# Kernel tuning notes

Measured on AMD Instinct MI355X. Metric: run time of the kernel, lower is better.

## Reference

```python
import jax, jax.numpy as jnp
import numpy as np

N = 100000      # nodes
E = 1600000     # edges (before self-loops)
F_IN = 128      # num_feats
H = 128         # dim_hidden
C = 64          # num_classes
EPS = 1e-5      # BatchNorm eps
SLOPE = 0.2     # LeakyReLU negative slope (PyG GATConv default)


def setup_inputs() -> dict:
    key = jax.random.key(0)
    ks = jax.random.split(key, 8)
    x = jax.random.normal(ks[0], (N, F_IN), jnp.float32)
    edge_index = jax.random.randint(ks[1], (2, E), 0, N, dtype=jnp.int32)
    W0 = jax.random.normal(ks[2], (F_IN, H), jnp.float32) * (1.0 / np.sqrt(F_IN))
    a_src0 = jax.random.normal(ks[3], (H,), jnp.float32) * 0.1
    a_dst0 = jax.random.normal(ks[4], (H,), jnp.float32) * 0.1
    W1 = jax.random.normal(ks[5], (H, C), jnp.float32) * (1.0 / np.sqrt(H))
    a_src1 = jax.random.normal(ks[6], (C,), jnp.float32) * 0.1
    a_dst1 = jax.random.normal(ks[7], (C,), jnp.float32) * 0.1
    return {
        "x": x, "edge_index": edge_index,
        "W0": W0, "a_src0": a_src0, "a_dst0": a_dst0,
        "g0": jnp.ones((H,), jnp.float32), "b0": jnp.zeros((H,), jnp.float32),
        "W1": W1, "a_src1": a_src1, "a_dst1": a_dst1,
        "g1": jnp.ones((C,), jnp.float32), "b1": jnp.zeros((C,), jnp.float32),
    }


def _gat_conv(x, src, dst, W, a_s, a_d):
    # x: [N, d_in]; src/dst: [E'] (self-loops included). heads=1, bias=False.
    h = x @ W                                   # [N, d_out]
    s = h @ a_s                                 # [N] alpha_src per node
    d = h @ a_d                                 # [N] alpha_dst per node
    logits = jax.nn.leaky_relu(s[src] + d[dst], SLOPE)   # [E']
    # segment softmax over incoming edges of each dst node
    m = jax.ops.segment_max(logits, dst, num_segments=N)
    w = jnp.exp(logits - m[dst])
    denom = jax.ops.segment_sum(w, dst, num_segments=N)
    coef = w / denom[dst]                       # [E']
    return jax.ops.segment_sum(coef[:, None] * h[src], dst, num_segments=N)


def _batch_norm(x, g, b):
    mu = jnp.mean(x, axis=0)
    var = jnp.var(x, axis=0)
    return (x - mu) * jax.lax.rsqrt(var + EPS) * g + b


def reference(x, edge_index, W0, a_src0, a_dst0, g0, b0, W1, a_src1, a_dst1, g1, b1):
    loops = jnp.arange(N, dtype=edge_index.dtype)
    src = jnp.concatenate([edge_index[0], loops])
    dst = jnp.concatenate([edge_index[1], loops])
    h = _gat_conv(x, src, dst, W0, a_src0, a_dst0)
    h = jax.nn.relu(_batch_norm(h, g0, b0))
    h = _gat_conv(h, src, dst, W1, a_src1, a_dst1)
    return jax.nn.relu(_batch_norm(h, g1, b1))
```

## Files before the change

kernel.cpp:

```cpp
#include <hip/hip_runtime.h>
#include <hip/hip_bf16.h>
#include <cmath>

#define BN_EPS 1e-5f
#define SLOPE 0.2f

typedef __attribute__((ext_vector_type(8))) short bf16x8;
typedef __attribute__((ext_vector_type(4))) float f32x4;

__device__ __forceinline__ float lrelu(float x) { return x >= 0.f ? x : SLOPE * x; }
__device__ __forceinline__ float bfl(unsigned u) { return __uint_as_float(u << 16); }
__device__ __forceinline__ float bfh(unsigned u) { return __uint_as_float(u & 0xffff0000u); }
__device__ __forceinline__ float bf2f(unsigned short u) { return __uint_as_float((unsigned)u << 16); }
__device__ __forceinline__ unsigned short f2bf(float f) {
    __hip_bfloat16 h = __float2bfloat16(f);
    return *reinterpret_cast<unsigned short*>(&h);
}

__global__ __launch_bounds__(512) void k_hist(const int* __restrict__ ei, int E, int n,
                                              int nbk, int* __restrict__ gcnt) {
    __shared__ int h[512];
    int t = threadIdx.x;
    for (int i = t; i < nbk; i += 512) h[i] = 0;
    __syncthreads();
    int base = blockIdx.x * 8192;
    int tot = E + n;
#pragma unroll
    for (int k = 0; k < 16; ++k) {
        int i = base + k * 512 + t;
        if (i < tot) {
            int dst = (i < E) ? ei[E + i] : (i - E);
            atomicAdd(&h[dst >> 8], 1);
        }
    }
    __syncthreads();
    for (int i = t; i < nbk; i += 512)
        if (h[i]) atomicAdd(&gcnt[i], h[i]);
}

__global__ __launch_bounds__(512) void k_bscan(const int* __restrict__ gcnt,
                                               int* __restrict__ gbase,
                                               int* __restrict__ gnext, int nbk) {
    __shared__ int tmp[512];
    int t = threadIdx.x;
    int v = (t < nbk) ? gcnt[t] : 0;
    tmp[t] = v;
    __syncthreads();
    for (int off = 1; off < 512; off <<= 1) {
        int a = (t >= off) ? tmp[t - off] : 0;
        __syncthreads();
        tmp[t] += a;
        __syncthreads();
    }
    int ex = tmp[t] - v;
    if (t < nbk) { gbase[t] = ex; gnext[t] = ex; }
    if (t == nbk - 1) gbase[nbk] = tmp[t];
}

__global__ __launch_bounds__(512) void k_bucket(const int* __restrict__ ei, int E, int n,
                                                int nbk, int* __restrict__ gnext,
                                                int2* __restrict__ bbuf) {
    __shared__ int h[512], off[512];
    int t = threadIdx.x;
    for (int i = t; i < nbk; i += 512) h[i] = 0;
    __syncthreads();
    int base = blockIdx.x * 8192;
    int tot = E + n;
    int srcv[16], dstv[16], rnk[16];
#pragma unroll
    for (int k = 0; k < 16; ++k) {
        int i = base + k * 512 + t;
        dstv[k] = -1;
        if (i < tot) {
            int s, d;
            if (i < E) { s = ei[i]; d = ei[E + i]; }
            else       { s = i - E; d = s; }
            srcv[k] = s; dstv[k] = d;
            rnk[k] = atomicAdd(&h[d >> 8], 1);
        }
    }
    __syncthreads();
    for (int i = t; i < nbk; i += 512)
        if (h[i]) off[i] = atomicAdd(&gnext[i], h[i]);
    __syncthreads();
#pragma unroll
    for (int k = 0; k < 16; ++k) {
        int d = dstv[k];
        if (d >= 0)
            bbuf[off[d >> 8] + rnk[k]] = make_int2(srcv[k], d);
    }
}

__global__ __launch_bounds__(256) void k_csr2(const int2* __restrict__ bbuf,
                                              const int* __restrict__ gbase,
                                              int* __restrict__ rowp, int* __restrict__ csr,
                                              int* __restrict__ dste, int n, int nbk) {
    __shared__ int cnt[256], scn[256];
    int b = blockIdx.x;
    int t = threadIdx.x;
    int beg = gbase[b], end = gbase[b + 1];
    int node0 = b << 8;
    cnt[t] = 0;
    __syncthreads();
    for (int i = beg + t; i < end; i += 256)
        atomicAdd(&cnt[bbuf[i].y & 255], 1);
    __syncthreads();
    int v = cnt[t];
    scn[t] = v;
    __syncthreads();
    for (int off = 1; off < 256; off <<= 1) {
        int a = (t >= off) ? scn[t - off] : 0;
        __syncthreads();
        scn[t] += a;
        __syncthreads();
    }
    int ex = scn[t] - v;
    if (node0 + t < n) rowp[node0 + t] = beg + ex;
    if (b == nbk - 1 && t == 0) rowp[n] = end;
    cnt[t] = ex;
    __syncthreads();
    for (int i = beg + t; i < end; i += 256) {
        int2 e = bbuf[i];
        int pos = atomicAdd(&cnt[e.y & 255], 1);
        csr[beg + pos] = e.x;
        dste[beg + pos] = e.y;
    }
}

__global__ __launch_bounds__(256) void k_coef(const int* __restrict__ csr,
                                              const int* __restrict__ dste,
                                              const float* __restrict__ s,
                                              const float* __restrict__ d,
                                              float* __restrict__ wv, int tot) {
    int e4 = (blockIdx.x * 256 + threadIdx.x) * 4;
    if (e4 + 3 < tot) {
        int4 c = *(const int4*)&csr[e4];
        int4 dd = *(const int4*)&dste[e4];
        float4 w;
        w.x = __expf(lrelu(s[c.x] + d[dd.x]));
        w.y = __expf(lrelu(s[c.y] + d[dd.y]));
        w.z = __expf(lrelu(s[c.z] + d[dd.z]));
        w.w = __expf(lrelu(s[c.w] + d[dd.w]));
        *(float4*)&wv[e4] = w;
    } else {
        for (int e = e4; e < tot; ++e)
            wv[e] = __expf(lrelu(s[csr[e]] + d[dste[e]]));
    }
}

__global__ void k_packw2(const float* __restrict__ W0, const float* __restrict__ W1,
                         unsigned short* __restrict__ Wp0, unsigned short* __restrict__ Wp1) {
    int idx = blockIdx.x * 256 + threadIdx.x;
    if (idx < 128 * 128) {
        int k = idx >> 7, nG = idx & 127;
        int nt = nG >> 4, nn = nG & 15, ks = k >> 5, g = (k >> 3) & 3, j = k & 7;
        Wp0[(((nt * 4 + ks) * 64) + g * 16 + nn) * 8 + j] = f2bf(W0[idx]);
    } else {
        int i2 = idx - 128 * 128;
        if (i2 < 128 * 64) {
            int k = i2 >> 6, nG = i2 & 63;
            int nt = nG >> 4, nn = nG & 15, ks = k >> 5, g = (k >> 3) & 3, j = k & 7;
            Wp1[(((nt * 4 + ks) * 64) + g * 16 + nn) * 8 + j] = f2bf(W1[i2]);
        }
    }
}

template <int CD, bool BN_IN, bool XBF>
__global__ __launch_bounds__(256) void k_gemm_mfma(
    const void* __restrict__ Xv, const unsigned short* __restrict__ Wp,
    const float* __restrict__ bnsums, const float* __restrict__ gg,
    const float* __restrict__ bb, const float* __restrict__ a_s,
    const float* __restrict__ a_d, unsigned short* __restrict__ hb,
    float* __restrict__ s_out, float* __restrict__ d_out, int n) {
    constexpr int NT = CD / 16;
    const float* Xf = (const float*)Xv;
    const unsigned short* Xh = (const unsigned short*)Xv;
    __shared__ unsigned short wl[128 * CD];
    __shared__ float sc[128], sh[128];
    int t = threadIdx.x;
    for (int i = t * 8; i < 128 * CD; i += 2048)
        *(uint4*)&wl[i] = *(const uint4*)&Wp[i];
    if constexpr (BN_IN) {
        if (t < 128) {
            float invn = 1.f / (float)n;
            float mu = bnsums[t] * invn;
            float var = bnsums[128 + t] * invn - mu * mu;
            float s = gg[t] * rsqrtf(var + BN_EPS);
            sc[t] = s;
            sh[t] = bb[t] - mu * s;
        }
    }
    __syncthreads();
    int w = t >> 6, l = t & 63;
    int m = l & 15, g = l >> 4;
    int r0 = blockIdx.x * 64;
    int row = r0 + w * 16 + m;
    bool rv = row < n;
    bf16x8 af[4];
#pragma unroll
    for (int ks = 0; ks < 4; ++ks) {
        int c0 = ks * 32 + g * 8;
        float xv[8];
        if constexpr (XBF) {
            uint4 u = make_uint4(0, 0, 0, 0);
            if (rv) u = *(const uint4*)&Xh[(size_t)row * 128 + c0];
            unsigned uu[4] = {u.x, u.y, u.z, u.w};
#pragma unroll
            for (int q = 0; q < 4; ++q) { xv[2 * q] = bfl(uu[q]); xv[2 * q + 1] = bfh(uu[q]); }
        } else {
            float4 x0 = make_float4(0.f, 0.f, 0.f, 0.f), x1 = x0;
            if (rv) {
                x0 = *(const float4*)&Xf[(size_t)row * 128 + c0];
                x1 = *(const float4*)&Xf[(size_t)row * 128 + c0 + 4];
            }
            xv[0] = x0.x; xv[1] = x0.y; xv[2] = x0.z; xv[3] = x0.w;
            xv[4] = x1.x; xv[5] = x1.y; xv[6] = x1.z; xv[7] = x1.w;
        }
        bf16x8 a;
#pragma unroll
        for (int j = 0; j < 8; ++j) {
            float v = xv[j];
            if constexpr (BN_IN) v = fmaxf(0.f, v * sc[c0 + j] + sh[c0 + j]);
            a[j] = (short)f2bf(v);
        }
        af[ks] = a;
    }
    f32x4 acc[NT];
#pragma unroll
    for (int i = 0; i < NT; ++i) acc[i] = (f32x4){0.f, 0.f, 0.f, 0.f};
#pragma unroll
    for (int ks = 0; ks < 4; ++ks) {
#pragma unroll
        for (int nt = 0; nt < NT; ++nt) {
            bf16x8 bfr = *(bf16x8*)&wl[(((nt * 4 + ks) * 64) + l) * 8];
            acc[nt] = __builtin_amdgcn_mfma_f32_16x16x32_bf16(af[ks], bfr, acc[nt], 0, 0, 0);
        }
    }
    float ps[4] = {0.f, 0.f, 0.f, 0.f}, pd[4] = {0.f, 0.f, 0.f, 0.f};
#pragma unroll
    for (int nt = 0; nt < NT; ++nt) {
        float as = a_s[nt * 16 + m], ad = a_d[nt * 16 + m];
#pragma unroll
        for (int r = 0; r < 4; ++r) {
            ps[r] += acc[nt][r] * as;
            pd[r] += acc[nt][r] * ad;
        }
    }
#pragma unroll
    for (int off = 1; off < 16; off <<= 1) {
#pragma unroll
        for (int r = 0; r < 4; ++r) {
            ps[r] += __shfl_xor(ps[r], off);
            pd[r] += __shfl_xor(pd[r], off);
        }
    }
    __syncthreads();
    unsigned short* ot = wl;
#pragma unroll
    for (int nt = 0; nt < NT; ++nt) {
#pragma unroll
        for (int r = 0; r < 4; ++r)
            ot[(w * 16 + g * 4 + r) * CD + nt * 16 + m] = f2bf(acc[nt][r]);
    }
    if (m == 0) {
        int orow = r0 + w * 16 + g * 4;
#pragma unroll
        for (int r = 0; r < 4; ++r) {
            if (orow + r < n) { s_out[orow + r] = ps[r]; d_out[orow + r] = pd[r]; }
        }
    }
    __syncthreads();
    constexpr int CPR = CD / 8;
    for (int c = t; c < 64 * CPR; c += 256) {
        int rr = c / CPR, cc = c % CPR;
        if (r0 + rr < n)
            *(uint4*)&hb[(size_t)(r0 + rr) * CD + cc * 8] = *(uint4*)&ot[rr * CD + cc * 8];
    }
}

template <int DIM, bool OUT_BF>
__global__ __launch_bounds__(256) void k_agg(
    const unsigned short* __restrict__ hb, const float* __restrict__ wv,
    const int* __restrict__ rowp, const int* __restrict__ csr,
    void* __restrict__ outv, int n) {
    constexpr int LPE = DIM / 8;
    int gid = blockIdx.x * blockDim.x + threadIdx.x;
    int wid = gid / LPE;
    int ll = gid & (LPE - 1);
    if (wid >= n) return;
    int beg = rowp[wid], end = rowp[wid + 1];
    float acc[8] = {};
    float denom = 0.f;
    int e = beg;
    for (; e + 3 < end; e += 4) {
        int i0 = csr[e], i1 = csr[e + 1], i2 = csr[e + 2], i3 = csr[e + 3];
        float w0 = wv[e], w1 = wv[e + 1], w2 = wv[e + 2], w3 = wv[e + 3];
        uint4 p0 = *(const uint4*)&hb[(size_t)i0 * DIM + ll * 8];
        uint4 p1 = *(const uint4*)&hb[(size_t)i1 * DIM + ll * 8];
        uint4 p2 = *(const uint4*)&hb[(size_t)i2 * DIM + ll * 8];
        uint4 p3 = *(const uint4*)&hb[(size_t)i3 * DIM + ll * 8];
        denom += (w0 + w1) + (w2 + w3);
        unsigned a0[4] = {p0.x, p0.y, p0.z, p0.w};
        unsigned a1[4] = {p1.x, p1.y, p1.z, p1.w};
        unsigned a2[4] = {p2.x, p2.y, p2.z, p2.w};
        unsigned a3[4] = {p3.x, p3.y, p3.z, p3.w};
#pragma unroll
        for (int q = 0; q < 4; ++q) {
            acc[2 * q]     += w0 * bfl(a0[q]) + w1 * bfl(a1[q]) + w2 * bfl(a2[q]) + w3 * bfl(a3[q]);
            acc[2 * q + 1] += w0 * bfh(a0[q]) + w1 * bfh(a1[q]) + w2 * bfh(a2[q]) + w3 * bfh(a3[q]);
        }
    }
    for (; e < end; ++e) {
        int i0 = csr[e];
        float w0 = wv[e];
        uint4 p0 = *(const uint4*)&hb[(size_t)i0 * DIM + ll * 8];
        unsigned a0[4] = {p0.x, p0.y, p0.z, p0.w};
        denom += w0;
#pragma unroll
        for (int q = 0; q < 4; ++q) {
            acc[2 * q]     += w0 * bfl(a0[q]);
            acc[2 * q + 1] += w0 * bfh(a0[q]);
        }
    }
    float inv = 1.f / denom;
    if constexpr (OUT_BF) {
        unsigned u[4];
#pragma unroll
        for (int q = 0; q < 4; ++q)
            u[q] = (unsigned)f2bf(acc[2 * q] * inv) |
                   ((unsigned)f2bf(acc[2 * q + 1] * inv) << 16);
        *(uint4*)((unsigned short*)outv + (size_t)wid * DIM + ll * 8) =
            make_uint4(u[0], u[1], u[2], u[3]);
    } else {
        float* orow = (float*)outv + (size_t)wid * DIM + ll * 8;
        *(float4*)&orow[0] = make_float4(acc[0] * inv, acc[1] * inv, acc[2] * inv, acc[3] * inv);
        *(float4*)&orow[4] = make_float4(acc[4] * inv, acc[5] * inv, acc[6] * inv, acc[7] * inv);
    }
}

template <int CD, bool XBF>
__global__ void k_bn_stats(const void* __restrict__ xv, float* __restrict__ sums, int n) {
    const float* xf = (const float*)xv;
    const unsigned short* xh = (const unsigned short*)xv;
    constexpr int RPB = 256 / CD;
    int t = threadIdx.x;
    int c = t & (CD - 1);
    int rl = t / CD;
    float s = 0.f, sq = 0.f;
    for (int r = blockIdx.x * RPB + rl; r < n; r += gridDim.x * RPB) {
        float v = XBF ? bf2f(xh[(size_t)r * CD + c]) : xf[(size_t)r * CD + c];
        s += v;
        sq += v * v;
    }
    __shared__ float ls[256], lq[256];
    ls[t] = s; lq[t] = sq;
    __syncthreads();
    if (t < CD) {
#pragma unroll
        for (int j = 1; j < RPB; ++j) { s += ls[t + j * CD]; sq += lq[t + j * CD]; }
        atomicAdd(&sums[c], s);
        atomicAdd(&sums[CD + c], sq);
    }
}

template <int CD>
__global__ void k_bn_apply(const float* __restrict__ x, const float* __restrict__ sums,
                           const float* __restrict__ g, const float* __restrict__ b,
                           float* __restrict__ out, int n) {
    size_t i = (size_t)blockIdx.x * blockDim.x + threadIdx.x;
    size_t tot = (size_t)n * CD;
    if (i >= tot) return;
    int c = (int)(i & (CD - 1));
    float invn = 1.f / (float)n;
    float mu = sums[c] * invn;
    float var = sums[CD + c] * invn - mu * mu;
    float v = (x[i] - mu) * rsqrtf(var + BN_EPS) * g[c] + b[c];
    out[i] = fmaxf(v, 0.f);
}

extern "C" void kernel_launch(void* const* d_in, const int* in_sizes, int n_in,
                              void* d_out, int out_size, void* d_ws, size_t ws_size,
                              hipStream_t stream) {
    const float* x   = (const float*)d_in[0];
    const int*   ei  = (const int*)  d_in[1];
    const float* W0  = (const float*)d_in[2];
    const float* as0 = (const float*)d_in[3];
    const float* ad0 = (const float*)d_in[4];
    const float* g0  = (const float*)d_in[5];
    const float* b0  = (const float*)d_in[6];
    const float* W1  = (const float*)d_in[7];
    const float* as1 = (const float*)d_in[8];
    const float* ad1 = (const float*)d_in[9];
    const float* g1  = (const float*)d_in[10];
    const float* b1  = (const float*)d_in[11];
    float* out = (float*)d_out;

    const int N_ = in_sizes[0] / 128;
    const int E_ = in_sizes[1] / 2;
    const int TOT = E_ + N_;
    const int nbk = (N_ + 255) >> 8;

    char* p = (char*)d_ws;
    unsigned short* hb   = (unsigned short*)p; p += (size_t)N_ * 128 * 2;
    unsigned short* aggB = (unsigned short*)p; p += (size_t)N_ * 128 * 2;
    float* agg1 = (float*)p;                   p += (size_t)N_ * 64 * 4;
    int2* bbuf  = (int2*)p;                    p += (size_t)TOT * 8;
    float* s0   = (float*)p;                   p += (size_t)N_ * 4;
    float* d0   = (float*)p;                   p += (size_t)N_ * 4;
    float* bns0 = (float*)p;                   p += 256 * 4;
    float* bns1 = (float*)p;                   p += 128 * 4;
    int* gcnt   = (int*)p;                     p += 512 * 4;
    int* gbase  = (int*)p;                     p += 514 * 4;
    int* gnext  = (int*)p;                     p += 512 * 4;
    int* rowp   = (int*)p;                     p += (size_t)(N_ + 2) * 4;
    int* csr    = (int*)p;                     p += (size_t)TOT * 4;
    int* dste   = (int*)p;                     p += (size_t)TOT * 4;
    float* wv   = (float*)p;                   p += (size_t)TOT * 4;
    unsigned short* Wp0 = (unsigned short*)p;  p += 128 * 128 * 2;
    unsigned short* Wp1 = (unsigned short*)p;  p += 128 * 64 * 2;

    hipMemsetAsync(gcnt, 0, 512 * 4, stream);
    hipMemsetAsync(bns0, 0, 384 * 4, stream);

    const int ebBlocks = (TOT + 8191) / 8192;
    k_hist<<<ebBlocks, 512, 0, stream>>>(ei, E_, N_, nbk, gcnt);
    k_bscan<<<1, 512, 0, stream>>>(gcnt, gbase, gnext, nbk);
    k_bucket<<<ebBlocks, 512, 0, stream>>>(ei, E_, N_, nbk, gnext, bbuf);
    k_csr2<<<nbk, 256, 0, stream>>>(bbuf, gbase, rowp, csr, dste, N_, nbk);

    k_packw2<<<96, 256, 0, stream>>>(W0, W1, Wp0, Wp1);

    const int gemmBlocks = (N_ + 63) / 64;
    const int aggBlocks128 = (N_ + 15) / 16;
    const int aggBlocks64  = (N_ + 31) / 32;
    const int coefBlocks   = (TOT + 1023) / 1024;

    k_gemm_mfma<128, false, false><<<gemmBlocks, 256, 0, stream>>>(
        x, Wp0, nullptr, nullptr, nullptr, as0, ad0, hb, s0, d0, N_);
    k_coef<<<coefBlocks, 256, 0, stream>>>(csr, dste, s0, d0, wv, TOT);
    k_agg<128, true><<<aggBlocks128, 256, 0, stream>>>(hb, wv, rowp, csr, aggB, N_);
    k_bn_stats<128, true><<<256, 256, 0, stream>>>(aggB, bns0, N_);

    k_gemm_mfma<64, true, true><<<gemmBlocks, 256, 0, stream>>>(
        aggB, Wp1, bns0, g0, b0, as1, ad1, hb, s0, d0, N_);
    k_coef<<<coefBlocks, 256, 0, stream>>>(csr, dste, s0, d0, wv, TOT);
    k_agg<64, false><<<aggBlocks64, 256, 0, stream>>>(hb, wv, rowp, csr, agg1, N_);
    k_bn_stats<64, false><<<256, 256, 0, stream>>>(agg1, bns1, N_);
    k_bn_apply<64><<<(int)(((size_t)N_ * 64 + 255) / 256), 256, 0, stream>>>(
        agg1, bns1, g1, b1, out, N_);
}
```

Baseline: 412.7 us.

## Fuse layer-0 edge coefficient computation into CSR build and unroll aggregation by eight

The first GEMM now runs before the CSR construction, so the CSR scatter kernel can compute the layer-0 exp(leaky_relu(s+d)) edge weights as it writes each edge. This removes one k_coef launch and the extra pass over csr/dste. The aggregation kernel also gets an 8-way unrolled gather loop, which keeps more independent row loads in flight at the cost of more registers. The s/d gathers inside k_csr2 are scattered accesses and add work to a kernel that was previously cheap.

```diff
diff --git a/kernel.cpp b/kernel.cpp
--- a/kernel.cpp
+++ b/kernel.cpp
@@ -94,7 +94,10 @@
 __global__ __launch_bounds__(256) void k_csr2(const int2* __restrict__ bbuf,
                                               const int* __restrict__ gbase,
                                               int* __restrict__ rowp, int* __restrict__ csr,
-                                              int* __restrict__ dste, int n, int nbk) {
+                                              int* __restrict__ dste,
+                                              const float* __restrict__ s,
+                                              const float* __restrict__ d,
+                                              float* __restrict__ wv, int n, int nbk) {
     __shared__ int cnt[256], scn[256];
     int b = blockIdx.x;
     int t = threadIdx.x;
@@ -124,6 +127,7 @@
         int pos = atomicAdd(&cnt[e.y & 255], 1);
         csr[beg + pos] = e.x;
         dste[beg + pos] = e.y;
+        wv[beg + pos] = __expf(lrelu(s[e.x] + d[e.y]));
     }
 }
 
@@ -289,31 +293,60 @@
     int ll = gid & (LPE - 1);
     if (wid >= n) return;
     int beg = rowp[wid], end = rowp[wid + 1];
+    const unsigned short* hbl = hb + ll * 8;
     float acc[8] = {};
     float denom = 0.f;
     int e = beg;
+    for (; e + 7 < end; e += 8) {
+        uint4 p[8];
+        float w8[8];
+#pragma unroll
+        for (int k = 0; k < 8; ++k) {
+            int idx = csr[e + k];
+            w8[k] = wv[e + k];
+            p[k] = *(const uint4*)&hbl[(size_t)idx * DIM];
+        }
+#pragma unroll
+        for (int k = 0; k < 8; ++k) denom += w8[k];
+#pragma unroll
+        for (int q = 0; q < 4; ++q) {
+            unsigned v0[8];
+#pragma unroll
+            for (int k = 0; k < 8; ++k) v0[k] = (q == 0) ? p[k].x : (q == 1) ? p[k].y : (q == 2) ? p[k].z : p[k].w;
+#pragma unroll
+            for (int k = 0; k < 8; ++k) {
+                acc[2 * q]     += w8[k] * bfl(v0[k]);
+                acc[2 * q + 1] += w8[k] * bfh(v0[k]);
+            }
+        }
+    }
     for (; e + 3 < end; e += 4) {
-        int i0 = csr[e], i1 = csr[e + 1], i2 = csr[e + 2], i3 = csr[e + 3];
-        float w0 = wv[e], w1 = wv[e + 1], w2 = wv[e + 2], w3 = wv[e + 3];
-        uint4 p0 = *(const uint4*)&hb[(size_t)i0 * DIM + ll * 8];
-        uint4 p1 = *(const uint4*)&hb[(size_t)i1 * DIM + ll * 8];
-        uint4 p2 = *(const uint4*)&hb[(size_t)i2 * DIM + ll * 8];
-        uint4 p3 = *(const uint4*)&hb[(size_t)i3 * DIM + ll * 8];
-        denom += (w0 + w1) + (w2 + w3);
-        unsigned a0[4] = {p0.x, p0.y, p0.z, p0.w};
-        unsigned a1[4] = {p1.x, p1.y, p1.z, p1.w};
-        unsigned a2[4] = {p2.x, p2.y, p2.z, p2.w};
-        unsigned a3[4] = {p3.x, p3.y, p3.z, p3.w};
+        uint4 p[4];
+        float w4[4];
+#pragma unroll
+        for (int k = 0; k < 4; ++k) {
+            int idx = csr[e + k];
+            w4[k] = wv[e + k];
+            p[k] = *(const uint4*)&hbl[(size_t)idx * DIM];
+        }
+#pragma unroll
+        for (int k = 0; k < 4; ++k) denom += w4[k];
 #pragma unroll
         for (int q = 0; q < 4; ++q) {
-            acc[2 * q]     += w0 * bfl(a0[q]) + w1 * bfl(a1[q]) + w2 * bfl(a2[q]) + w3 * bfl(a3[q]);
-            acc[2 * q + 1] += w0 * bfh(a0[q]) + w1 * bfh(a1[q]) + w2 * bfh(a2[q]) + w3 * bfh(a3[q]);
+            unsigned v0[4];
+#pragma unroll
+            for (int k = 0; k < 4; ++k) v0[k] = (q == 0) ? p[k].x : (q == 1) ? p[k].y : (q == 2) ? p[k].z : p[k].w;
+#pragma unroll
+            for (int k = 0; k < 4; ++k) {
+                acc[2 * q]     += w4[k] * bfl(v0[k]);
+                acc[2 * q + 1] += w4[k] * bfh(v0[k]);
+            }
         }
     }
     for (; e < end; ++e) {
         int i0 = csr[e];
         float w0 = wv[e];
-        uint4 p0 = *(const uint4*)&hb[(size_t)i0 * DIM + ll * 8];
+        uint4 p0 = *(const uint4*)&hbl[(size_t)i0 * DIM];
         unsigned a0[4] = {p0.x, p0.y, p0.z, p0.w};
         denom += w0;
 #pragma unroll
@@ -422,22 +455,21 @@
     hipMemsetAsync(gcnt, 0, 512 * 4, stream);
     hipMemsetAsync(bns0, 0, 384 * 4, stream);
 
-    const int ebBlocks = (TOT + 8191) / 8192;
-    k_hist<<<ebBlocks, 512, 0, stream>>>(ei, E_, N_, nbk, gcnt);
-    k_bscan<<<1, 512, 0, stream>>>(gcnt, gbase, gnext, nbk);
-    k_bucket<<<ebBlocks, 512, 0, stream>>>(ei, E_, N_, nbk, gnext, bbuf);
-    k_csr2<<<nbk, 256, 0, stream>>>(bbuf, gbase, rowp, csr, dste, N_, nbk);
-
-    k_packw2<<<96, 256, 0, stream>>>(W0, W1, Wp0, Wp1);
-
     const int gemmBlocks = (N_ + 63) / 64;
     const int aggBlocks128 = (N_ + 15) / 16;
     const int aggBlocks64  = (N_ + 31) / 32;
     const int coefBlocks   = (TOT + 1023) / 1024;
-
+    const int ebBlocks = (TOT + 8191) / 8192;
+
+    k_packw2<<<96, 256, 0, stream>>>(W0, W1, Wp0, Wp1);
     k_gemm_mfma<128, false, false><<<gemmBlocks, 256, 0, stream>>>(
         x, Wp0, nullptr, nullptr, nullptr, as0, ad0, hb, s0, d0, N_);
-    k_coef<<<coefBlocks, 256, 0, stream>>>(csr, dste, s0, d0, wv, TOT);
+
+    k_hist<<<ebBlocks, 512, 0, stream>>>(ei, E_, N_, nbk, gcnt);
+    k_bscan<<<1, 512, 0, stream>>>(gcnt, gbase, gnext, nbk);
+    k_bucket<<<ebBlocks, 512, 0, stream>>>(ei, E_, N_, nbk, gnext, bbuf);
+    k_csr2<<<nbk, 256, 0, stream>>>(bbuf, gbase, rowp, csr, dste, s0, d0, wv, N_, nbk);
+
     k_agg<128, true><<<aggBlocks128, 256, 0, stream>>>(hb, wv, rowp, csr, aggB, N_);
     k_bn_stats<128, true><<<256, 256, 0, stream>>>(aggB, bns0, N_);
 
```

Result: slower. 425.1 us (+3.0%).
